# Kernel tuning notes

Hardware: AMD Instinct MI355X
Metric: run time of the kernel (lower is better)

Reference implementation:

```python
import jax, jax.numpy as jnp
import numpy as np

H = 8          # n_heads
LORA_SCALE = 1.0


def _lora(x, down, up):
    # nn.Linear convention: y = x @ W.T ; down:[r,in], up:[out,r]
    return (x @ down.T) @ up.T


def setup_inputs() -> dict:
    key = jax.random.key(0)
    ks = jax.random.split(key, 16)
    B, S, D, R = 4, 2048, 640, 4
    std = 1.0 / np.sqrt(D)
    inp = {
        "hidden_states": jax.random.normal(ks[0], (B, S, D), jnp.float32),
        "wq": jax.random.normal(ks[1], (D, D), jnp.float32) * std,
        "wk": jax.random.normal(ks[2], (D, D), jnp.float32) * std,
        "wv": jax.random.normal(ks[3], (D, D), jnp.float32) * std,
        "wo": jax.random.normal(ks[4], (D, D), jnp.float32) * std,
        "bo": jax.random.normal(ks[5], (D,), jnp.float32) * 0.02,
        "q_down": jax.random.normal(ks[6], (R, D), jnp.float32) * (1.0 / R),
        "q_up": jax.random.normal(ks[7], (D, R), jnp.float32) * 0.02,
        "k_down": jax.random.normal(ks[8], (R, D), jnp.float32) * (1.0 / R),
        "k_up": jax.random.normal(ks[9], (D, R), jnp.float32) * 0.02,
        "v_down": jax.random.normal(ks[10], (R, D), jnp.float32) * (1.0 / R),
        "v_up": jax.random.normal(ks[11], (D, R), jnp.float32) * 0.02,
        "o_down": jax.random.normal(ks[12], (R, D), jnp.float32) * (1.0 / R),
        "o_up": jax.random.normal(ks[13], (D, R), jnp.float32) * 0.02,
    }
    return inp


def reference(hidden_states, wq, wk, wv, wo, bo,
              q_down, q_up, k_down, k_up, v_down, v_up, o_down, o_up):
    B, S, D = hidden_states.shape
    hd = D // H
    sm_scale = 1.0 / np.sqrt(hd)

    x = hidden_states  # self-attention: encoder_hidden_states = hidden_states
    q = x @ wq.T + LORA_SCALE * _lora(x, q_down, q_up)
    k = x @ wk.T + LORA_SCALE * _lora(x, k_down, k_up)
    v = x @ wv.T + LORA_SCALE * _lora(x, v_down, v_up)

    # head_to_batch_dim: [B,S,D] -> [B,H,S,hd]
    q = q.reshape(B, S, H, hd).transpose(0, 2, 1, 3)
    k = k.reshape(B, S, H, hd).transpose(0, 2, 1, 3)
    v = v.reshape(B, S, H, hd).transpose(0, 2, 1, 3)

    # get_attention_scores: baddbmm(beta=0, alpha=1/sqrt(hd)) + softmax
    scores = jnp.einsum("bhqd,bhkd->bhqk", q, k) * sm_scale
    probs = jax.nn.softmax(scores, axis=-1)
    attn_out = jnp.einsum("bhqk,bhkd->bhqd", probs, v)

    # batch_to_head_dim: [B,H,S,hd] -> [B,S,D]
    attn_out = attn_out.transpose(0, 2, 1, 3).reshape(B, S, D)

    # out projection (with bias) + LoRA on the pre-projection hidden states
    out = attn_out @ wo.T + bo + LORA_SCALE * _lora(attn_out, o_down, o_up)
    # to_out[1] is dropout -> identity at eval
    return out
```

## Files before the change

### kernel.cpp

```cpp
#include <hip/hip_runtime.h>

typedef unsigned short u16;
typedef unsigned int u32;
typedef unsigned long long u64;

typedef __bf16 bf16x8 __attribute__((ext_vector_type(8)));
typedef float f32x4 __attribute__((ext_vector_type(4)));
typedef float f32x16 __attribute__((ext_vector_type(16)));

__device__ __forceinline__ float b2f(u16 u) {
    union { u32 i; float f; } c; c.i = ((u32)u) << 16; return c.f;
}
__device__ __forceinline__ u16 f2b(float f) {
    union { float f; u32 i; } c; c.f = f;
    u32 r = c.i + 0x7fffu + ((c.i >> 16) & 1u);
    return (u16)(r >> 16);
}
__device__ __forceinline__ u32 pack2(float a, float b) {
    return (u32)f2b(a) | ((u32)f2b(b) << 16);
}
__device__ __forceinline__ u32 cvt_pk_bf16(float a, float b) {
    u32 r;
    asm("v_cvt_pk_bf16_f32 %0, %1, %2" : "=v"(r) : "v"(a), "v"(b));
    return r;
}
__device__ __forceinline__ float fexp2(float x) {
    float r;
    asm("v_exp_f32 %0, %1" : "=v"(r) : "v"(x));
    return r;
}

__device__ __forceinline__ f32x4 mfma16(bf16x8 a, bf16x8 b, f32x4 c) {
    return __builtin_amdgcn_mfma_f32_16x16x32_bf16(a, b, c, 0, 0, 0);
}
__device__ __forceinline__ f32x16 mfma32(bf16x8 a, bf16x8 b, f32x16 c) {
    return __builtin_amdgcn_mfma_f32_32x32x16_bf16(a, b, c, 0, 0, 0);
}

__device__ __forceinline__ void lds_cp16(const u16* gsrc, u16* ldst) {
    __builtin_amdgcn_global_load_lds(
        (const __attribute__((address_space(1))) u32*)gsrc,
        (__attribute__((address_space(3))) u32*)ldst, 16, 0, 0);
}

struct ConvJobs {
    const float* s[4];
    u16* d[4];
};

__global__ __launch_bounds__(256) void prep(ConvJobs J,
                                            const float* __restrict__ x,
                                            const float* __restrict__ qd,
                                            const float* __restrict__ kd,
                                            const float* __restrict__ vd,
                                            u16* __restrict__ xb,
                                            float* __restrict__ T,
                                            u16* __restrict__ vt, int do_pad) {
    int bx = blockIdx.x;
    if (bx < 1600) {
        int j = bx / 400;
        int i = (bx - j * 400) * 256 + threadIdx.x;
        float4 v = ((const float4*)J.s[j])[i];
        ushort4 o;
        o.x = f2b(v.x); o.y = f2b(v.y); o.z = f2b(v.z); o.w = f2b(v.w);
        ((ushort4*)J.d[j])[i] = o;
    } else if (bx < 3648) {
        int m = (bx - 1600) * 4 + (threadIdx.x >> 6);
        int lane = threadIdx.x & 63;
        const float* row = x + (size_t)m * 640;
        u16* orow = xb + (size_t)m * 640;
        float acc[12];
#pragma unroll
        for (int r = 0; r < 12; ++r) acc[r] = 0.f;
#pragma unroll
        for (int ii = 0; ii < 10; ++ii) {
            int i = lane + ii * 64;
            float a = row[i];
            orow[i] = f2b(a);
#pragma unroll
            for (int r = 0; r < 4; ++r) {
                acc[r]     += a * qd[r * 640 + i];
                acc[4 + r] += a * kd[r * 640 + i];
                acc[8 + r] += a * vd[r * 640 + i];
            }
        }
#pragma unroll
        for (int off = 32; off > 0; off >>= 1)
#pragma unroll
            for (int r = 0; r < 12; ++r) acc[r] += __shfl_xor(acc[r], off);
        if (lane == 0) {
#pragma unroll
            for (int p = 0; p < 3; ++p) {
                float4* t = (float4*)(T + ((size_t)p * 8192 + m) * 4);
                *t = make_float4(acc[p * 4], acc[p * 4 + 1], acc[p * 4 + 2],
                                 acc[p * 4 + 3]);
            }
        }
    } else if (do_pad) {
        int idx = (bx - 3648) * 256 + threadIdx.x;
        int q = idx * 4;
        int bh = q >> 15;
        int rem = q & 32767;
        int row = rem >> 11, col = rem & 2047;
        u16 val = (row == 0) ? (u16)0x3F80 : (u16)0;
        ushort4 o = make_ushort4(val, val, val, val);
        *(ushort4*)(vt + ((size_t)bh * 96 + 80 + row) * 2048 + col) = o;
    }
}

__global__ __launch_bounds__(256) void lora_down_o(const u16* __restrict__ A,
                                                   const float* __restrict__ dn,
                                                   float* __restrict__ T) {
    int m = blockIdx.x * 4 + (threadIdx.x >> 6);
    int lane = threadIdx.x & 63;
    const u16* arow = A + (size_t)m * 640;
    float a0 = 0.f, a1 = 0.f, a2 = 0.f, a3 = 0.f;
    for (int i = lane; i < 640; i += 64) {
        float a = b2f(arow[i]);
        a0 += a * dn[i];
        a1 += a * dn[640 + i];
        a2 += a * dn[1280 + i];
        a3 += a * dn[1920 + i];
    }
#pragma unroll
    for (int off = 32; off > 0; off >>= 1) {
        a0 += __shfl_xor(a0, off);
        a1 += __shfl_xor(a1, off);
        a2 += __shfl_xor(a2, off);
        a3 += __shfl_xor(a3, off);
    }
    if (lane == 0) {
        float4* t = (float4*)(T + (size_t)m * 4);
        *t = make_float4(a0, a1, a2, a3);
    }
}

struct QkvPtrs {
    const u16* W[3];
    const float* up[3];
    void* out[3];
    float scale[3];
    int mode[3];
};

__global__ __launch_bounds__(256) void gemm_bt(const u16* __restrict__ A, QkvPtrs P,
                                               const float* __restrict__ T,
                                               const float* __restrict__ bias) {
    int z = blockIdx.z;
    const u16* W = P.W[z];
    const float* up = P.up[z];
    const float scl = P.scale[z];
    const int md = P.mode[z];
    const float* Tz = T + (size_t)z * 8192 * 4;
    int m0 = blockIdx.x * 128, n0 = blockIdx.y * 128;
    int tid = threadIdx.x, lane = tid & 63, wid = tid >> 6;
    int g = lane >> 4, l15 = lane & 15;
    __shared__ __align__(16) u16 smem[24576];
    u16* As_ = smem;
    u16* Bs_ = smem + 12288;
    f32x4 acc[4][4] = {};
    int wm = (wid & 1) * 64, wn = (wid >> 1) * 64;

    int r0 = tid >> 2, cb = (tid & 3) * 8;
    const u16* pA = A + (size_t)(m0 + r0) * 640 + cb;
    const u16* pB = W + (size_t)(n0 + r0) * 640 + cb;

    auto stage = [&](int buf, int k0) {
        u16* da = As_ + buf * 4096 + tid * 8;
        u16* db = Bs_ + buf * 4096 + tid * 8;
        lds_cp16(pA + k0, da);
        lds_cp16(pA + 40960 + k0, da + 2048);
        lds_cp16(pB + k0, db);
        lds_cp16(pB + 40960 + k0, db + 2048);
    };
    auto compute = [&](int cur) {
        const u16* as = As_ + cur * 4096;
        const u16* bs = Bs_ + cur * 4096;
        bf16x8 af[4], bfv[4];
#pragma unroll
        for (int q4 = 0; q4 < 4; ++q4) {
            af[q4]  = *(const bf16x8*)(as + (wm + q4 * 16 + l15) * 32 + g * 8);
            bfv[q4] = *(const bf16x8*)(bs + (wn + q4 * 16 + l15) * 32 + g * 8);
        }
#pragma unroll
        for (int i = 0; i < 4; ++i)
#pragma unroll
            for (int j = 0; j < 4; ++j)
                acc[i][j] = mfma16(af[i], bfv[j], acc[i][j]);
    };

    stage(0, 0);
    stage(1, 32);
    int cur = 0;
    for (int t = 0; t < 19; ++t) {
        asm volatile("s_waitcnt vmcnt(4)" ::: "memory");
        __builtin_amdgcn_s_barrier();
        asm volatile("" ::: "memory");
        if (t < 18) stage((cur == 0) ? 2 : cur - 1, (t + 2) * 32);
        compute(cur);
        cur = (cur == 2) ? 0 : cur + 1;
    }
    asm volatile("s_waitcnt vmcnt(0)" ::: "memory");
    __builtin_amdgcn_s_barrier();
    asm volatile("" ::: "memory");
    compute(cur);

    float4 upv[4];
    float bv[4];
#pragma unroll
    for (int j = 0; j < 4; ++j) {
        int n = n0 + wn + j * 16 + l15;
        upv[j] = *(const float4*)(up + n * 4);
        bv[j] = (md == 1) ? bias[n] : 0.f;
    }

    if (md == 2) {
        __syncthreads();
        u16* Tl = smem;
#pragma unroll
        for (int i = 0; i < 4; ++i) {
#pragma unroll
            for (int j = 0; j < 4; ++j) {
                float vs[4];
#pragma unroll
                for (int r = 0; r < 4; ++r) {
                    int m = m0 + wm + i * 16 + g * 4 + r;
                    const float4 tv = *(const float4*)(Tz + (size_t)m * 4);
                    vs[r] = acc[i][j][r] + tv.x * upv[j].x + tv.y * upv[j].y +
                            tv.z * upv[j].z + tv.w * upv[j].w;
                }
                uint2 pk;
                pk.x = pack2(vs[0], vs[1]);
                pk.y = pack2(vs[2], vs[3]);
                *(uint2*)(Tl + (wn + j * 16 + l15) * 136 + wm + i * 16 + g * 4) = pk;
            }
        }
        __syncthreads();
        int bb2 = m0 >> 11;
        int sl0 = m0 & 2047;
        u16* outb_ = (u16*)P.out[z];
#pragma unroll
        for (int it = 0; it < 16; ++it) {
            int qq = it * 256 + tid;
            int row = qq >> 5;
            int pos = (qq & 31) * 4;
            int ss = (pos & ~12) | ((pos & 4) << 1) | ((pos & 8) >> 1);
            uint2 val = *(const uint2*)(Tl + row * 136 + ss);
            int n = n0 + row;
            int h = n / 80, d = n - h * 80;
            *(uint2*)(outb_ + (((size_t)bb2 * 8 + h) * 96 + d) * 2048 + sl0 + pos) = val;
        }
        return;
    }

    float* outf = (float*)P.out[z];
    u16* outb = (u16*)P.out[z];
#pragma unroll
    for (int i = 0; i < 4; ++i) {
#pragma unroll
        for (int r = 0; r < 4; ++r) {
            int m = m0 + wm + i * 16 + g * 4 + r;
            const float4 tv = *(const float4*)(Tz + (size_t)m * 4);
#pragma unroll
            for (int j = 0; j < 4; ++j) {
                int n = n0 + wn + j * 16 + l15;
                float v = acc[i][j][r] + tv.x * upv[j].x + tv.y * upv[j].y +
                          tv.z * upv[j].z + tv.w * upv[j].w + bv[j];
                if (md == 1) {
                    outf[(size_t)m * 640 + n] = v;
                } else {
                    int bb = m >> 11, s = m & 2047;
                    int h = n / 80, d = n - h * 80;
                    outb[(((size_t)bb * 8 + h) * 2048 + s) * 80 + d] = f2b(v * scl);
                }
            }
        }
    }
}

__global__ __launch_bounds__(256) void transpose_v(const u16* __restrict__ Vin,
                                                   u16* __restrict__ Vout) {
    __shared__ u32 lds32[64 * 41];
    int bh = blockIdx.y;
    int s0 = blockIdx.x * 64;
    int tid = threadIdx.x;
    const u16* in = Vin + (size_t)bh * 2048 * 80;
    u16* out = Vout + (size_t)bh * 96 * 2048;

    for (int t = tid; t < 640; t += 256) {
        int s = t / 10, c = t - s * 10;
        uint4 v = *(const uint4*)(in + (size_t)(s0 + s) * 80 + c * 8);
        u32* p = lds32 + s * 41 + c * 4;
        p[0] = v.x; p[1] = v.y; p[2] = v.z; p[3] = v.w;
    }
    __syncthreads();
    for (int t = tid; t < 640; t += 256) {
        int d = t >> 3, c8 = t & 7;
        int dp = d >> 1, hi = d & 1;
        u16 vals[8];
#pragma unroll
        for (int j = 0; j < 8; ++j) {
            u32 w = lds32[(c8 * 8 + j) * 41 + dp];
            vals[j] = hi ? (u16)(w >> 16) : (u16)(w & 0xffff);
        }
        u16* dst = out + (size_t)d * 2048 + s0 + (c8 >> 1) * 16 + (c8 & 1) * 4;
        *(uint2*)dst = *(const uint2*)(vals);
        *(uint2*)(dst + 8) = *(const uint2*)(vals + 4);
    }
    for (int t = tid; t < 1024; t += 256) {
        int r = t >> 6, c = t & 63;
        out[(size_t)(80 + r) * 2048 + s0 + c] = (r == 0) ? 0x3F80 : 0;
    }
}

__global__ __launch_bounds__(512) void flash_attn(const u16* __restrict__ Q,
                                                  const u16* __restrict__ K,
                                                  const u16* __restrict__ Vt_g,
                                                  u16* __restrict__ O) {
    int bh = blockIdx.y;
    int q0 = blockIdx.x * 256;
    int tid = threadIdx.x;
    int lane = tid & 63, wid = tid >> 6, l31 = lane & 31, h2 = lane >> 5;
    const size_t base = (size_t)bh * 2048 * 80;
    const size_t vbase = (size_t)bh * 96 * 2048;

    __shared__ __align__(16) u16 lds[2 * 5632 + 2 * 7200];
    u16* Ks0 = lds;
    u16* Vt0 = lds + 11264;

    bf16x8 qf[5];
    {
        int qrow = q0 + wid * 32 + l31;
#pragma unroll
        for (int ks = 0; ks < 5; ++ks)
            qf[ks] = *(const bf16x8*)(Q + base + (size_t)qrow * 80 + ks * 16 + h2 * 8);
    }

    f32x16 oa[3] = {};
    const float C2 = 17.312340490667562f;

    auto stage = [&](int buf, int kt) {
#pragma unroll
        for (int it = 0; it < 4; ++it) {
            int c = tid + it * 512;
            if (c < 704) {
                int row = c / 11, col = c - row * 11;
                lds_cp16(K + base + (size_t)(kt + row) * 80 + col * 8,
                         Ks0 + buf * 5632 + c * 8);
            } else if (c < 1600) {
                int t = c - 704;
                int row = t / 9, col = t - row * 9;
                lds_cp16(Vt_g + vbase + (size_t)row * 2048 + kt + col * 8,
                         Vt0 + buf * 7200 + t * 8);
            }
        }
    };

    stage(0, 0);
    __syncthreads();

    for (int i = 0; i < 32; ++i) {
        int cur = i & 1;
        if (i < 31) stage(cur ^ 1, (i + 1) * 64);

        const u16* ks = Ks0 + cur * 5632;
        const u16* vt = Vt0 + cur * 7200;

#pragma unroll
        for (int kk2 = 0; kk2 < 2; ++kk2) {
            f32x16 s = {};
            __builtin_amdgcn_s_setprio(1);
#pragma unroll
            for (int ks5 = 0; ks5 < 5; ++ks5) {
                bf16x8 kf = *(const bf16x8*)(ks + (kk2 * 32 + l31) * 88 + ks5 * 16 + h2 * 8);
                s = mfma32(kf, qf[ks5], s);
            }
            __builtin_amdgcn_s_setprio(0);
            u32 d[8];
#pragma unroll
            for (int j = 0; j < 8; ++j)
                d[j] = cvt_pk_bf16(fexp2(s[2 * j] - C2), fexp2(s[2 * j + 1] - C2));
            __builtin_amdgcn_s_setprio(1);
#pragma unroll
            for (int sl = 0; sl < 2; ++sl) {
                union { u32 w[4]; bf16x8 v; } pa;
                pa.w[0] = d[4 * sl + 0];
                pa.w[1] = d[4 * sl + 1];
                pa.w[2] = d[4 * sl + 2];
                pa.w[3] = d[4 * sl + 3];
#pragma unroll
                for (int nt = 0; nt < 3; ++nt) {
                    bf16x8 vf = *(const bf16x8*)(vt + (nt * 32 + l31) * 72 +
                                                 kk2 * 32 + sl * 16 + h2 * 8);
                    oa[nt] = mfma32(pa.v, vf, oa[nt]);
                }
            }
            __builtin_amdgcn_s_setprio(0);
        }
        __syncthreads();
    }

    int b = bh >> 3, h = bh & 7;
    float inv[16];
#pragma unroll
    for (int reg = 0; reg < 16; ++reg)
        inv[reg] = 1.f / __shfl(oa[2][reg], (lane & 32) + 16, 64);
#pragma unroll
    for (int nt = 0; nt < 3; ++nt) {
        int vd = nt * 32 + l31;
        if (vd < 80) {
#pragma unroll
            for (int reg = 0; reg < 16; ++reg) {
                int q = q0 + wid * 32 + (reg & 3) + 8 * (reg >> 2) + 4 * h2;
                O[((size_t)(b * 2048 + q)) * 640 + h * 80 + vd] = f2b(oa[nt][reg] * inv[reg]);
            }
        }
    }
}

extern "C" void kernel_launch(void* const* d_in, const int* in_sizes, int n_in,
                              void* d_out, int out_size, void* d_ws, size_t ws_size,
                              hipStream_t stream) {
    const float* x      = (const float*)d_in[0];
    const float* wq     = (const float*)d_in[1];
    const float* wk     = (const float*)d_in[2];
    const float* wv     = (const float*)d_in[3];
    const float* wo     = (const float*)d_in[4];
    const float* bo     = (const float*)d_in[5];
    const float* q_down = (const float*)d_in[6];
    const float* q_up   = (const float*)d_in[7];
    const float* k_down = (const float*)d_in[8];
    const float* k_up   = (const float*)d_in[9];
    const float* v_down = (const float*)d_in[10];
    const float* v_up   = (const float*)d_in[11];
    const float* o_down = (const float*)d_in[12];
    const float* o_up   = (const float*)d_in[13];

    char* ws = (char*)d_ws;
    u16* xb    = (u16*)(ws);
    u16* wbv   = (u16*)(ws + 10485760);
    u16* wbq   = (u16*)(ws + 11304960);
    u16* wbk   = (u16*)(ws + 12124160);
    u16* wbo   = (u16*)(ws + 12943360);
    u16* q_ws  = (u16*)(ws + 13762560);
    u16* k_ws  = (u16*)(ws + 24248320);
    u16* v_ws  = (u16*)(ws + 34734080);
    u16* attn  = (u16*)(ws + 45219840);
    float* Tq  = (float*)(ws + 55705600);
    float* To  = (float*)(ws + 56098816);

    const size_t vt_off = 56360960;
    const size_t vt_need = vt_off + 12582912 + 16384;
    const bool direct_vt = (ws_size >= vt_need);
    u16* vT_ws = direct_vt ? (u16*)(ws + vt_off)
                           : (u16*)(ws);

    ConvJobs cj;
    cj.s[0] = wq; cj.d[0] = wbq;
    cj.s[1] = wk; cj.d[1] = wbk;
    cj.s[2] = wv; cj.d[2] = wbv;
    cj.s[3] = wo; cj.d[3] = wbo;
    prep<<<4672, 256, 0, stream>>>(cj, x, q_down, k_down, v_down, xb, Tq,
                                   vT_ws, direct_vt ? 1 : 0);

    QkvPtrs pq;
    pq.W[0] = wbq; pq.W[1] = wbk; pq.W[2] = wbv;
    pq.up[0] = q_up; pq.up[1] = k_up; pq.up[2] = v_up;
    pq.out[0] = q_ws; pq.out[1] = k_ws;
    pq.out[2] = direct_vt ? (void*)vT_ws : (void*)v_ws;
    pq.scale[0] = 0.11180339887498949f * 1.4426950408889634f;
    pq.scale[1] = 1.0f;
    pq.scale[2] = 1.0f;
    pq.mode[0] = 0; pq.mode[1] = 0; pq.mode[2] = direct_vt ? 2 : 0;
    gemm_bt<<<dim3(64, 5, 3), 256, 0, stream>>>(xb, pq, Tq, bo);

    if (!direct_vt)
        transpose_v<<<dim3(32, 32), 256, 0, stream>>>(v_ws, vT_ws);

    flash_attn<<<dim3(8, 32), 512, 0, stream>>>(q_ws, k_ws, vT_ws, attn);

    lora_down_o<<<2048, 256, 0, stream>>>(attn, o_down, To);

    QkvPtrs po;
    po.W[0] = wbo; po.W[1] = wbo; po.W[2] = wbo;
    po.up[0] = o_up; po.up[1] = o_up; po.up[2] = o_up;
    po.out[0] = d_out; po.out[1] = d_out; po.out[2] = d_out;
    po.scale[0] = 1.0f; po.scale[1] = 1.0f; po.scale[2] = 1.0f;
    po.mode[0] = 1; po.mode[1] = 1; po.mode[2] = 1;
    gemm_bt<<<dim3(64, 5, 1), 256, 0, stream>>>(attn, po, To, bo);
}
```

Baseline: 213.2 us.

## Fold LoRA up·down products into merged bf16 projection weights

Computes W + up·down per weight during the fp32-to-bf16 weight conversion, so each projection becomes a single GEMM. This removes the per-row LoRA down-projection work in prep, the separate lora_down_o kernel, and the rank-4 epilogue corrections in the GEMMs, saving one launch and some memory traffic. The LoRA delta is now rounded to bf16 together with the base weight rather than applied in fp32, which slightly changes numerics.

After: 193.8 us, median of 3. 9.1% less time.

```diff
diff --git a/kernel.cpp b/kernel.cpp
--- a/kernel.cpp
+++ b/kernel.cpp
@@ -45,59 +45,46 @@
 
 struct ConvJobs {
     const float* s[4];
+    const float* up[4];
+    const float* dn[4];
     u16* d[4];
 };
 
 __global__ __launch_bounds__(256) void prep(ConvJobs J,
                                             const float* __restrict__ x,
-                                            const float* __restrict__ qd,
-                                            const float* __restrict__ kd,
-                                            const float* __restrict__ vd,
                                             u16* __restrict__ xb,
-                                            float* __restrict__ T,
                                             u16* __restrict__ vt, int do_pad) {
     int bx = blockIdx.x;
     if (bx < 1600) {
         int j = bx / 400;
         int i = (bx - j * 400) * 256 + threadIdx.x;
-        float4 v = ((const float4*)J.s[j])[i];
+        int n = i / 160;
+        int k4 = (i - n * 160) * 4;
+        float4 w = ((const float4*)J.s[j])[i];
+        float4 u = *(const float4*)(J.up[j] + n * 4);
+        const float* dnp = J.dn[j];
+        float4 d0 = *(const float4*)(dnp + k4);
+        float4 d1 = *(const float4*)(dnp + 640 + k4);
+        float4 d2 = *(const float4*)(dnp + 1280 + k4);
+        float4 d3 = *(const float4*)(dnp + 1920 + k4);
         ushort4 o;
-        o.x = f2b(v.x); o.y = f2b(v.y); o.z = f2b(v.z); o.w = f2b(v.w);
+        o.x = f2b(w.x + u.x * d0.x + u.y * d1.x + u.z * d2.x + u.w * d3.x);
+        o.y = f2b(w.y + u.x * d0.y + u.y * d1.y + u.z * d2.y + u.w * d3.y);
+        o.z = f2b(w.z + u.x * d0.z + u.y * d1.z + u.z * d2.z + u.w * d3.z);
+        o.w = f2b(w.w + u.x * d0.w + u.y * d1.w + u.z * d2.w + u.w * d3.w);
         ((ushort4*)J.d[j])[i] = o;
-    } else if (bx < 3648) {
-        int m = (bx - 1600) * 4 + (threadIdx.x >> 6);
-        int lane = threadIdx.x & 63;
-        const float* row = x + (size_t)m * 640;
-        u16* orow = xb + (size_t)m * 640;
-        float acc[12];
-#pragma unroll
-        for (int r = 0; r < 12; ++r) acc[r] = 0.f;
-#pragma unroll
-        for (int ii = 0; ii < 10; ++ii) {
-            int i = lane + ii * 64;
-            float a = row[i];
-            orow[i] = f2b(a);
-#pragma unroll
-            for (int r = 0; r < 4; ++r) {
-                acc[r]     += a * qd[r * 640 + i];
-                acc[4 + r] += a * kd[r * 640 + i];
-                acc[8 + r] += a * vd[r * 640 + i];
-            }
-        }
-#pragma unroll
-        for (int off = 32; off > 0; off >>= 1)
-#pragma unroll
-            for (int r = 0; r < 12; ++r) acc[r] += __shfl_xor(acc[r], off);
-        if (lane == 0) {
-#pragma unroll
-            for (int p = 0; p < 3; ++p) {
-                float4* t = (float4*)(T + ((size_t)p * 8192 + m) * 4);
-                *t = make_float4(acc[p * 4], acc[p * 4 + 1], acc[p * 4 + 2],
-                                 acc[p * 4 + 3]);
-            }
+    } else if (bx < 2880) {
+        int base = (bx - 1600) * 1024 + threadIdx.x;
+#pragma unroll
+        for (int it = 0; it < 4; ++it) {
+            int i = base + it * 256;
+            float4 v = ((const float4*)x)[i];
+            ushort4 o;
+            o.x = f2b(v.x); o.y = f2b(v.y); o.z = f2b(v.z); o.w = f2b(v.w);
+            ((ushort4*)xb)[i] = o;
         }
     } else if (do_pad) {
-        int idx = (bx - 3648) * 256 + threadIdx.x;
+        int idx = (bx - 2880) * 256 + threadIdx.x;
         int q = idx * 4;
         int bh = q >> 15;
         int rem = q & 32767;
@@ -108,50 +95,19 @@
     }
 }
 
-__global__ __launch_bounds__(256) void lora_down_o(const u16* __restrict__ A,
-                                                   const float* __restrict__ dn,
-                                                   float* __restrict__ T) {
-    int m = blockIdx.x * 4 + (threadIdx.x >> 6);
-    int lane = threadIdx.x & 63;
-    const u16* arow = A + (size_t)m * 640;
-    float a0 = 0.f, a1 = 0.f, a2 = 0.f, a3 = 0.f;
-    for (int i = lane; i < 640; i += 64) {
-        float a = b2f(arow[i]);
-        a0 += a * dn[i];
-        a1 += a * dn[640 + i];
-        a2 += a * dn[1280 + i];
-        a3 += a * dn[1920 + i];
-    }
-#pragma unroll
-    for (int off = 32; off > 0; off >>= 1) {
-        a0 += __shfl_xor(a0, off);
-        a1 += __shfl_xor(a1, off);
-        a2 += __shfl_xor(a2, off);
-        a3 += __shfl_xor(a3, off);
-    }
-    if (lane == 0) {
-        float4* t = (float4*)(T + (size_t)m * 4);
-        *t = make_float4(a0, a1, a2, a3);
-    }
-}
-
 struct QkvPtrs {
     const u16* W[3];
-    const float* up[3];
     void* out[3];
     float scale[3];
     int mode[3];
 };
 
 __global__ __launch_bounds__(256) void gemm_bt(const u16* __restrict__ A, QkvPtrs P,
-                                               const float* __restrict__ T,
                                                const float* __restrict__ bias) {
     int z = blockIdx.z;
     const u16* W = P.W[z];
-    const float* up = P.up[z];
     const float scl = P.scale[z];
     const int md = P.mode[z];
-    const float* Tz = T + (size_t)z * 8192 * 4;
     int m0 = blockIdx.x * 128, n0 = blockIdx.y * 128;
     int tid = threadIdx.x, lane = tid & 63, wid = tid >> 6;
     int g = lane >> 4, l15 = lane & 15;
@@ -205,12 +161,10 @@
     asm volatile("" ::: "memory");
     compute(cur);
 
-    float4 upv[4];
     float bv[4];
 #pragma unroll
     for (int j = 0; j < 4; ++j) {
         int n = n0 + wn + j * 16 + l15;
-        upv[j] = *(const float4*)(up + n * 4);
         bv[j] = (md == 1) ? bias[n] : 0.f;
     }
 
@@ -221,17 +175,9 @@
         for (int i = 0; i < 4; ++i) {
 #pragma unroll
             for (int j = 0; j < 4; ++j) {
-                float vs[4];
-#pragma unroll
-                for (int r = 0; r < 4; ++r) {
-                    int m = m0 + wm + i * 16 + g * 4 + r;
-                    const float4 tv = *(const float4*)(Tz + (size_t)m * 4);
-                    vs[r] = acc[i][j][r] + tv.x * upv[j].x + tv.y * upv[j].y +
-                            tv.z * upv[j].z + tv.w * upv[j].w;
-                }
                 uint2 pk;
-                pk.x = pack2(vs[0], vs[1]);
-                pk.y = pack2(vs[2], vs[3]);
+                pk.x = pack2(acc[i][j][0], acc[i][j][1]);
+                pk.y = pack2(acc[i][j][2], acc[i][j][3]);
                 *(uint2*)(Tl + (wn + j * 16 + l15) * 136 + wm + i * 16 + g * 4) = pk;
             }
         }
@@ -260,12 +206,10 @@
 #pragma unroll
         for (int r = 0; r < 4; ++r) {
             int m = m0 + wm + i * 16 + g * 4 + r;
-            const float4 tv = *(const float4*)(Tz + (size_t)m * 4);
 #pragma unroll
             for (int j = 0; j < 4; ++j) {
                 int n = n0 + wn + j * 16 + l15;
-                float v = acc[i][j][r] + tv.x * upv[j].x + tv.y * upv[j].y +
-                          tv.z * upv[j].z + tv.w * upv[j].w + bv[j];
+                float v = acc[i][j][r] + bv[j];
                 if (md == 1) {
                     outf[(size_t)m * 640 + n] = v;
                 } else {
@@ -446,8 +390,6 @@
     u16* k_ws  = (u16*)(ws + 24248320);
     u16* v_ws  = (u16*)(ws + 34734080);
     u16* attn  = (u16*)(ws + 45219840);
-    float* Tq  = (float*)(ws + 55705600);
-    float* To  = (float*)(ws + 56098816);
 
     const size_t vt_off = 56360960;
     const size_t vt_need = vt_off + 12582912 + 16384;
@@ -456,36 +398,31 @@
                            : (u16*)(ws);
 
     ConvJobs cj;
-    cj.s[0] = wq; cj.d[0] = wbq;
-    cj.s[1] = wk; cj.d[1] = wbk;
-    cj.s[2] = wv; cj.d[2] = wbv;
-    cj.s[3] = wo; cj.d[3] = wbo;
-    prep<<<4672, 256, 0, stream>>>(cj, x, q_down, k_down, v_down, xb, Tq,
-                                   vT_ws, direct_vt ? 1 : 0);
+    cj.s[0] = wq; cj.up[0] = q_up; cj.dn[0] = q_down; cj.d[0] = wbq;
+    cj.s[1] = wk; cj.up[1] = k_up; cj.dn[1] = k_down; cj.d[1] = wbk;
+    cj.s[2] = wv; cj.up[2] = v_up; cj.dn[2] = v_down; cj.d[2] = wbv;
+    cj.s[3] = wo; cj.up[3] = o_up; cj.dn[3] = o_down; cj.d[3] = wbo;
+    prep<<<3904, 256, 0, stream>>>(cj, x, xb, vT_ws, direct_vt ? 1 : 0);
 
     QkvPtrs pq;
     pq.W[0] = wbq; pq.W[1] = wbk; pq.W[2] = wbv;
-    pq.up[0] = q_up; pq.up[1] = k_up; pq.up[2] = v_up;
     pq.out[0] = q_ws; pq.out[1] = k_ws;
     pq.out[2] = direct_vt ? (void*)vT_ws : (void*)v_ws;
     pq.scale[0] = 0.11180339887498949f * 1.4426950408889634f;
     pq.scale[1] = 1.0f;
     pq.scale[2] = 1.0f;
     pq.mode[0] = 0; pq.mode[1] = 0; pq.mode[2] = direct_vt ? 2 : 0;
-    gemm_bt<<<dim3(64, 5, 3), 256, 0, stream>>>(xb, pq, Tq, bo);
+    gemm_bt<<<dim3(64, 5, 3), 256, 0, stream>>>(xb, pq, bo);
 
     if (!direct_vt)
         transpose_v<<<dim3(32, 32), 256, 0, stream>>>(v_ws, vT_ws);
 
     flash_attn<<<dim3(8, 32), 512, 0, stream>>>(q_ws, k_ws, vT_ws, attn);
 
-    lora_down_o<<<2048, 256, 0, stream>>>(attn, o_down, To);
-
     QkvPtrs po;
     po.W[0] = wbo; po.W[1] = wbo; po.W[2] = wbo;
-    po.up[0] = o_up; po.up[1] = o_up; po.up[2] = o_up;
     po.out[0] = d_out; po.out[1] = d_out; po.out[2] = d_out;
     po.scale[0] = 1.0f; po.scale[1] = 1.0f; po.scale[2] = 1.0f;
     po.mode[0] = 1; po.mode[1] = 1; po.mode[2] = 1;
-    gemm_bt<<<dim3(64, 5, 1), 256, 0, stream>>>(attn, po, To, bo);
-}
+    gemm_bt<<<dim3(64, 5, 1), 256, 0, stream>>>(attn, po, bo);
+}
```
